# Performance work log

Hardware: AMD Instinct MI355X
Metric: run time of the kernel (lower is better)

## Reference

```python
import jax, jax.numpy as jnp
import numpy as np

B, S, D, N, TOPK = 2, 2048, 4096, 8, 2


def setup_inputs() -> dict:
    key = jax.random.key(0)
    k1, k2, k3, k4, k5 = jax.random.split(key, 5)
    return {
        "x": jax.random.normal(k1, (B, S, D), dtype=jnp.float32),
        "base_res": jax.random.normal(k2, (B, S, D), dtype=jnp.float32),
        "lora_results": jax.random.normal(k3, (B, S, D, N), dtype=jnp.float32),
        "gate_W": jax.random.normal(k4, (N, D), dtype=jnp.float32) * 0.02,
        "gate_b": jax.random.normal(k5, (N,), dtype=jnp.float32) * 0.02,
        "top_k": TOPK,
    }


def reference(x, base_res, lora_results, gate_W, gate_b, top_k):
    # Pool last token: [B, D]
    pooled = x[:, -1, :]
    # All per-adapter Linear(D,1) gates fused into one matmul: [B, N]
    gate_weights = jnp.einsum("bd,nd->bn", pooled, gate_W) + gate_b
    # Top-k adapter selection (add_noise=False / eval mode)
    _, adapter_index = jax.lax.top_k(gate_weights, top_k)  # [B, k]
    # Gather along adapter dim (dim 3): [B, S, D, k]
    idx = adapter_index[:, None, None, :]  # broadcast over S, D
    activated_res = jnp.take_along_axis(lora_results, idx, axis=3)
    # Sum over selected adapters and add residual (note: gate weights are NOT
    # multiplied in, matching the original module's math).
    return base_res + jnp.sum(activated_res, axis=-1)
```

## Files before the change

### kernel.cpp

```cpp
#include <hip/hip_runtime.h>
#include <hip/hip_bf16.h>

#define B_SZ 2
#define S_SZ 2048
#define D_SZ 4096
#define N_ADP 8

__global__ void moe_gate_topk(const float* __restrict__ x,
                              const float* __restrict__ gate_W,
                              const float* __restrict__ gate_b,
                              const int* __restrict__ top_k_p,
                              float* __restrict__ w_out) {
    const int b = blockIdx.x;
    const float* xrow = x + ((size_t)b * S_SZ + (S_SZ - 1)) * D_SZ;

    float acc[N_ADP];
#pragma unroll
    for (int n = 0; n < N_ADP; ++n) acc[n] = 0.f;

    for (int d = threadIdx.x; d < D_SZ; d += blockDim.x) {
        const float xv = xrow[d];
#pragma unroll
        for (int n = 0; n < N_ADP; ++n)
            acc[n] += xv * gate_W[n * D_SZ + d];
    }

#pragma unroll
    for (int n = 0; n < N_ADP; ++n) {
#pragma unroll
        for (int off = 32; off > 0; off >>= 1)
            acc[n] += __shfl_down(acc[n], off, 64);
    }

    __shared__ float red[N_ADP][4];
    const int wave = threadIdx.x >> 6;
    const int lane = threadIdx.x & 63;
    if (lane == 0) {
#pragma unroll
        for (int n = 0; n < N_ADP; ++n) red[n][wave] = acc[n];
    }
    __syncthreads();

    if (threadIdx.x == 0) {
        const int nwaves = (int)(blockDim.x >> 6);
        float g[N_ADP];
#pragma unroll
        for (int n = 0; n < N_ADP; ++n) {
            float s = 0.f;
            for (int w = 0; w < nwaves; ++w) s += red[n][w];
            g[n] = s + gate_b[n];
        }
        float wsel[N_ADP];
#pragma unroll
        for (int n = 0; n < N_ADP; ++n) wsel[n] = 0.f;

        const int k = *top_k_p;
        for (int t = 0; t < k && t < N_ADP; ++t) {
            int best = -1;
            float bv = 0.f;
            for (int n = 0; n < N_ADP; ++n) {
                if (wsel[n] == 0.f && (best < 0 || g[n] > bv)) {
                    bv = g[n];
                    best = n;
                }
            }
            wsel[best] = 1.f;
        }
#pragma unroll
        for (int n = 0; n < N_ADP; ++n) w_out[b * N_ADP + n] = wsel[n];
    }
}

__global__ void moe_aggregate(const float* __restrict__ base,
                              const float* __restrict__ lora,
                              const float* __restrict__ w_ws,
                              float* __restrict__ out) {
    const int b = blockIdx.y;

    const float w0 = w_ws[b * N_ADP + 0];
    const float w1 = w_ws[b * N_ADP + 1];
    const float w2 = w_ws[b * N_ADP + 2];
    const float w3 = w_ws[b * N_ADP + 3];
    const float w4 = w_ws[b * N_ADP + 4];
    const float w5 = w_ws[b * N_ADP + 5];
    const float w6 = w_ws[b * N_ADP + 6];
    const float w7 = w_ws[b * N_ADP + 7];

    const size_t batch_elems = (size_t)S_SZ * D_SZ;
    const size_t batch_off = (size_t)b * batch_elems;
    const int ngroups = (int)(batch_elems / 4);

    const int stride = gridDim.x * blockDim.x;
    for (int g = blockIdx.x * blockDim.x + threadIdx.x; g < ngroups; g += stride) {
        const size_t e = batch_off + (size_t)g * 4;
        const float4 bv = *reinterpret_cast<const float4*>(base + e);
        const float4* lp = reinterpret_cast<const float4*>(lora + e * N_ADP);

        float4 ov;
        float* ovp = reinterpret_cast<float*>(&ov);
        const float* bvp = reinterpret_cast<const float*>(&bv);
#pragma unroll
        for (int j = 0; j < 4; ++j) {
            const float4 l0 = lp[2 * j];
            const float4 l1 = lp[2 * j + 1];
            float s = bvp[j];
            s += w0 * l0.x + w1 * l0.y + w2 * l0.z + w3 * l0.w;
            s += w4 * l1.x + w5 * l1.y + w6 * l1.z + w7 * l1.w;
            ovp[j] = s;
        }
        *reinterpret_cast<float4*>(out + e) = ov;
    }
}

extern "C" void kernel_launch(void* const* d_in, const int* in_sizes, int n_in,
                              void* d_out, int out_size, void* d_ws, size_t ws_size,
                              hipStream_t stream) {
    const float* x        = (const float*)d_in[0];
    const float* base_res = (const float*)d_in[1];
    const float* lora     = (const float*)d_in[2];
    const float* gate_W   = (const float*)d_in[3];
    const float* gate_b   = (const float*)d_in[4];
    const int*   top_k    = (const int*)d_in[5];
    float* out = (float*)d_out;
    float* w_ws = (float*)d_ws;

    moe_gate_topk<<<dim3(B_SZ), dim3(256), 0, stream>>>(x, gate_W, gate_b, top_k, w_ws);

    dim3 grid(2048, B_SZ);
    moe_aggregate<<<grid, dim3(256), 0, stream>>>(base_res, lora, w_ws, out);
}
```

Measured before the change: 143.1 us.

## Coalesce lora loads via per-wave LDS transpose with XOR swizzle

The aggregate kernel now has each wave load a contiguous 8 KB tile of lora with fully coalesced float4 loads. It stages the tile through a swizzled LDS buffer, then each lane reads back its 8 float4s to produce one output float4. Before, each lane read 128 contiguous bytes, which gave strided per-instruction access. The change also shrinks the grid to 512x2 and doubles the gate kernel block size with unrolling. It adds LDS traffic and per-wave staging, and the overall kernel stays bound by DRAM bandwidth.

```diff
diff --git a/kernel.cpp b/kernel.cpp
--- a/kernel.cpp
+++ b/kernel.cpp
@@ -18,6 +18,7 @@
 #pragma unroll
     for (int n = 0; n < N_ADP; ++n) acc[n] = 0.f;
 
+#pragma unroll 4
     for (int d = threadIdx.x; d < D_SZ; d += blockDim.x) {
         const float xv = xrow[d];
 #pragma unroll
@@ -32,7 +33,7 @@
             acc[n] += __shfl_down(acc[n], off, 64);
     }
 
-    __shared__ float red[N_ADP][4];
+    __shared__ float red[N_ADP][8];
     const int wave = threadIdx.x >> 6;
     const int lane = threadIdx.x & 63;
     if (lane == 0) {
@@ -71,44 +72,60 @@
     }
 }
 
-__global__ void moe_aggregate(const float* __restrict__ base,
-                              const float* __restrict__ lora,
-                              const float* __restrict__ w_ws,
-                              float* __restrict__ out) {
+__global__ __launch_bounds__(256) void moe_aggregate(
+        const float4* __restrict__ base4,
+        const float4* __restrict__ lora4,
+        const float* __restrict__ w_ws,
+        float4* __restrict__ out4) {
+    __shared__ float4 lds[4][512];
+
+    const int wv = threadIdx.x >> 6;
+    const int lane = threadIdx.x & 63;
     const int b = blockIdx.y;
 
-    const float w0 = w_ws[b * N_ADP + 0];
-    const float w1 = w_ws[b * N_ADP + 1];
-    const float w2 = w_ws[b * N_ADP + 2];
-    const float w3 = w_ws[b * N_ADP + 3];
-    const float w4 = w_ws[b * N_ADP + 4];
-    const float w5 = w_ws[b * N_ADP + 5];
-    const float w6 = w_ws[b * N_ADP + 6];
-    const float w7 = w_ws[b * N_ADP + 7];
+    const float* wp = w_ws + b * N_ADP;
+    const float w0 = wp[0], w1 = wp[1], w2 = wp[2], w3 = wp[3];
+    const float w4 = wp[4], w5 = wp[5], w6 = wp[6], w7 = wp[7];
 
-    const size_t batch_elems = (size_t)S_SZ * D_SZ;
-    const size_t batch_off = (size_t)b * batch_elems;
-    const int ngroups = (int)(batch_elems / 4);
+    const size_t loraq_batch = (size_t)S_SZ * D_SZ * (N_ADP / 4);
+    const size_t outq_batch  = (size_t)S_SZ * D_SZ / 4;
+    const float4* lbase = lora4 + (size_t)b * loraq_batch;
+    const float4* bbase = base4 + (size_t)b * outq_batch;
+    float4*       obase = out4  + (size_t)b * outq_batch;
 
-    const int stride = gridDim.x * blockDim.x;
-    for (int g = blockIdx.x * blockDim.x + threadIdx.x; g < ngroups; g += stride) {
-        const size_t e = batch_off + (size_t)g * 4;
-        const float4 bv = *reinterpret_cast<const float4*>(base + e);
-        const float4* lp = reinterpret_cast<const float4*>(lora + e * N_ADP);
+    const int tiles   = (int)(loraq_batch / 512);
+    const int wstride = gridDim.x * 4;
+
+    for (int t = blockIdx.x * 4 + wv; t < tiles; t += wstride) {
+        const size_t qbase = (size_t)t * 512;
+
+        float4 v[8];
+#pragma unroll
+        for (int r = 0; r < 8; ++r)
+            v[r] = lbase[qbase + (size_t)r * 64 + lane];
+
+#pragma unroll
+        for (int r = 0; r < 8; ++r)
+            lds[wv][(r * 64 + lane) ^ ((lane >> 3) & 7)] = v[r];
+
+        const size_t o = qbase / 8 + lane;
+        const float4 bv = bbase[o];
+
+        float4 q[8];
+#pragma unroll
+        for (int j = 0; j < 8; ++j)
+            q[j] = lds[wv][(8 * lane + j) ^ (lane & 7)];
 
         float4 ov;
-        float* ovp = reinterpret_cast<float*>(&ov);
-        const float* bvp = reinterpret_cast<const float*>(&bv);
-#pragma unroll
-        for (int j = 0; j < 4; ++j) {
-            const float4 l0 = lp[2 * j];
-            const float4 l1 = lp[2 * j + 1];
-            float s = bvp[j];
-            s += w0 * l0.x + w1 * l0.y + w2 * l0.z + w3 * l0.w;
-            s += w4 * l1.x + w5 * l1.y + w6 * l1.z + w7 * l1.w;
-            ovp[j] = s;
-        }
-        *reinterpret_cast<float4*>(out + e) = ov;
+        ov.x = bv.x + w0 * q[0].x + w1 * q[0].y + w2 * q[0].z + w3 * q[0].w
+                    + w4 * q[1].x + w5 * q[1].y + w6 * q[1].z + w7 * q[1].w;
+        ov.y = bv.y + w0 * q[2].x + w1 * q[2].y + w2 * q[2].z + w3 * q[2].w
+                    + w4 * q[3].x + w5 * q[3].y + w6 * q[3].z + w7 * q[3].w;
+        ov.z = bv.z + w0 * q[4].x + w1 * q[4].y + w2 * q[4].z + w3 * q[4].w
+                    + w4 * q[5].x + w5 * q[5].y + w6 * q[5].z + w7 * q[5].w;
+        ov.w = bv.w + w0 * q[6].x + w1 * q[6].y + w2 * q[6].z + w3 * q[6].w
+                    + w4 * q[7].x + w5 * q[7].y + w6 * q[7].z + w7 * q[7].w;
+        obase[o] = ov;
     }
 }
 
@@ -121,11 +138,12 @@
     const float* gate_W   = (const float*)d_in[3];
     const float* gate_b   = (const float*)d_in[4];
     const int*   top_k    = (const int*)d_in[5];
-    float* out = (float*)d_out;
+    float* out  = (float*)d_out;
     float* w_ws = (float*)d_ws;
 
-    moe_gate_topk<<<dim3(B_SZ), dim3(256), 0, stream>>>(x, gate_W, gate_b, top_k, w_ws);
+    moe_gate_topk<<<dim3(B_SZ), dim3(512), 0, stream>>>(x, gate_W, gate_b, top_k, w_ws);
 
-    dim3 grid(2048, B_SZ);
-    moe_aggregate<<<grid, dim3(256), 0, stream>>>(base_res, lora, w_ws, out);
+    dim3 grid(512, B_SZ);
+    moe_aggregate<<<grid, dim3(256), 0, stream>>>(
+        (const float4*)base_res, (const float4*)lora, w_ws, (float4*)out);
 }
```

Result: no change. 141.0 us (-1.5%).

## Parallelize gate dot per adapter, move top-k into aggregate, use nontemporal loads

Applied to the files above, without the earlier changes.

The gate kernel now runs one block per (adapter, batch) pair with float4 loads, so the serial 2-block gate launch gets more parallelism. Top-k selection moves into each aggregate thread, which reads the raw gate scores and bias from the workspace. The aggregate kernel uses nontemporal loads and stores for the streaming lora, base and output tensors, with half the grid and launch bounds. It still reads all 8 adapters' data densely, and every thread redundantly recomputes the top-k.

```diff
diff --git a/kernel.cpp b/kernel.cpp
--- a/kernel.cpp
+++ b/kernel.cpp
@@ -6,109 +6,97 @@
 #define D_SZ 4096
 #define N_ADP 8
 
-__global__ void moe_gate_topk(const float* __restrict__ x,
-                              const float* __restrict__ gate_W,
-                              const float* __restrict__ gate_b,
-                              const int* __restrict__ top_k_p,
-                              float* __restrict__ w_out) {
-    const int b = blockIdx.x;
-    const float* xrow = x + ((size_t)b * S_SZ + (S_SZ - 1)) * D_SZ;
+typedef float f4_t __attribute__((ext_vector_type(4)));
 
-    float acc[N_ADP];
+__global__ void moe_gate_dot(const f4_t* __restrict__ x4,
+                             const f4_t* __restrict__ gateW4,
+                             float* __restrict__ g_out) {
+    const int n = blockIdx.x;
+    const int b = blockIdx.y;
+    const f4_t* xrow = x4 + ((size_t)b * S_SZ + (S_SZ - 1)) * (D_SZ / 4);
+    const f4_t* wrow = gateW4 + (size_t)n * (D_SZ / 4);
+
+    float s = 0.f;
 #pragma unroll
-    for (int n = 0; n < N_ADP; ++n) acc[n] = 0.f;
-
-    for (int d = threadIdx.x; d < D_SZ; d += blockDim.x) {
-        const float xv = xrow[d];
-#pragma unroll
-        for (int n = 0; n < N_ADP; ++n)
-            acc[n] += xv * gate_W[n * D_SZ + d];
+    for (int i = 0; i < D_SZ / 4 / 256; ++i) {
+        const int d4 = i * 256 + threadIdx.x;
+        const f4_t xv = xrow[d4];
+        const f4_t wv = wrow[d4];
+        s += xv.x * wv.x + xv.y * wv.y + xv.z * wv.z + xv.w * wv.w;
     }
 
 #pragma unroll
-    for (int n = 0; n < N_ADP; ++n) {
-#pragma unroll
-        for (int off = 32; off > 0; off >>= 1)
-            acc[n] += __shfl_down(acc[n], off, 64);
-    }
+    for (int off = 32; off > 0; off >>= 1)
+        s += __shfl_down(s, off, 64);
 
-    __shared__ float red[N_ADP][4];
+    __shared__ float red[4];
     const int wave = threadIdx.x >> 6;
     const int lane = threadIdx.x & 63;
-    if (lane == 0) {
+    if (lane == 0) red[wave] = s;
+    __syncthreads();
+    if (threadIdx.x == 0)
+        g_out[b * N_ADP + n] = red[0] + red[1] + red[2] + red[3];
+}
+
+__global__ __launch_bounds__(256, 4) void moe_aggregate(
+        const f4_t* __restrict__ base4,
+        const f4_t* __restrict__ lora4,
+        const float* __restrict__ g_ws,
+        const float* __restrict__ gate_b,
+        const int* __restrict__ top_k_p,
+        f4_t* __restrict__ out4) {
+    const int b = blockIdx.y;
+
+    float g[N_ADP];
 #pragma unroll
-        for (int n = 0; n < N_ADP; ++n) red[n][wave] = acc[n];
-    }
-    __syncthreads();
+    for (int n = 0; n < N_ADP; ++n) g[n] = g_ws[b * N_ADP + n] + gate_b[n];
 
-    if (threadIdx.x == 0) {
-        const int nwaves = (int)(blockDim.x >> 6);
-        float g[N_ADP];
+    float w[N_ADP];
 #pragma unroll
-        for (int n = 0; n < N_ADP; ++n) {
-            float s = 0.f;
-            for (int w = 0; w < nwaves; ++w) s += red[n][w];
-            g[n] = s + gate_b[n];
-        }
-        float wsel[N_ADP];
-#pragma unroll
-        for (int n = 0; n < N_ADP; ++n) wsel[n] = 0.f;
-
+    for (int n = 0; n < N_ADP; ++n) w[n] = 0.f;
+    {
         const int k = *top_k_p;
         for (int t = 0; t < k && t < N_ADP; ++t) {
             int best = -1;
             float bv = 0.f;
+#pragma unroll
             for (int n = 0; n < N_ADP; ++n) {
-                if (wsel[n] == 0.f && (best < 0 || g[n] > bv)) {
+                if (w[n] == 0.f && (best < 0 || g[n] > bv)) {
                     bv = g[n];
                     best = n;
                 }
             }
-            wsel[best] = 1.f;
+            w[best] = 1.f;
         }
-#pragma unroll
-        for (int n = 0; n < N_ADP; ++n) w_out[b * N_ADP + n] = wsel[n];
     }
-}
+    const float w0 = w[0], w1 = w[1], w2 = w[2], w3 = w[3];
+    const float w4 = w[4], w5 = w[5], w6 = w[6], w7 = w[7];
 
-__global__ void moe_aggregate(const float* __restrict__ base,
-                              const float* __restrict__ lora,
-                              const float* __restrict__ w_ws,
-                              float* __restrict__ out) {
-    const int b = blockIdx.y;
-
-    const float w0 = w_ws[b * N_ADP + 0];
-    const float w1 = w_ws[b * N_ADP + 1];
-    const float w2 = w_ws[b * N_ADP + 2];
-    const float w3 = w_ws[b * N_ADP + 3];
-    const float w4 = w_ws[b * N_ADP + 4];
-    const float w5 = w_ws[b * N_ADP + 5];
-    const float w6 = w_ws[b * N_ADP + 6];
-    const float w7 = w_ws[b * N_ADP + 7];
-
-    const size_t batch_elems = (size_t)S_SZ * D_SZ;
-    const size_t batch_off = (size_t)b * batch_elems;
-    const int ngroups = (int)(batch_elems / 4);
+    const size_t outq_batch = (size_t)S_SZ * D_SZ / 4;
+    const size_t obase_off = (size_t)b * outq_batch;
+    const int nq = (int)outq_batch;
 
     const int stride = gridDim.x * blockDim.x;
-    for (int g = blockIdx.x * blockDim.x + threadIdx.x; g < ngroups; g += stride) {
-        const size_t e = batch_off + (size_t)g * 4;
-        const float4 bv = *reinterpret_cast<const float4*>(base + e);
-        const float4* lp = reinterpret_cast<const float4*>(lora + e * N_ADP);
+    for (int q = blockIdx.x * blockDim.x + threadIdx.x; q < nq; q += stride) {
+        const size_t o = obase_off + (size_t)q;
+        const f4_t bv = __builtin_nontemporal_load(base4 + o);
+        const f4_t* lp = lora4 + o * N_ADP;
 
-        float4 ov;
-        float* ovp = reinterpret_cast<float*>(&ov);
-        const float* bvp = reinterpret_cast<const float*>(&bv);
+        f4_t l[8];
 #pragma unroll
-        for (int j = 0; j < 4; ++j) {
-            const float4 l0 = lp[2 * j];
-            const float4 l1 = lp[2 * j + 1];
-            float s = bvp[j];
-            s += w0 * l0.x + w1 * l0.y + w2 * l0.z + w3 * l0.w;
-            s += w4 * l1.x + w5 * l1.y + w6 * l1.z + w7 * l1.w;
-            ovp[j] = s;
-        }
-        *reinterpret_cast<float4*>(out + e) = ov;
+        for (int j = 0; j < 8; ++j)
+            l[j] = __builtin_nontemporal_load(lp + j);
+
+        f4_t ov;
+        ov.x = bv.x + w0 * l[0].x + w1 * l[0].y + w2 * l[0].z + w3 * l[0].w
+                    + w4 * l[1].x + w5 * l[1].y + w6 * l[1].z + w7 * l[1].w;
+        ov.y = bv.y + w0 * l[2].x + w1 * l[2].y + w2 * l[2].z + w3 * l[2].w
+                    + w4 * l[3].x + w5 * l[3].y + w6 * l[3].z + w7 * l[3].w;
+        ov.z = bv.z + w0 * l[4].x + w1 * l[4].y + w2 * l[4].z + w3 * l[4].w
+                    + w4 * l[5].x + w5 * l[5].y + w6 * l[5].z + w7 * l[5].w;
+        ov.w = bv.w + w0 * l[6].x + w1 * l[6].y + w2 * l[6].z + w3 * l[6].w
+                    + w4 * l[7].x + w5 * l[7].y + w6 * l[7].z + w7 * l[7].w;
+        __builtin_nontemporal_store(ov, out4 + o);
     }
 }
 
@@ -121,11 +109,13 @@
     const float* gate_W   = (const float*)d_in[3];
     const float* gate_b   = (const float*)d_in[4];
     const int*   top_k    = (const int*)d_in[5];
-    float* out = (float*)d_out;
-    float* w_ws = (float*)d_ws;
+    float* out  = (float*)d_out;
+    float* g_ws = (float*)d_ws;
 
-    moe_gate_topk<<<dim3(B_SZ), dim3(256), 0, stream>>>(x, gate_W, gate_b, top_k, w_ws);
+    moe_gate_dot<<<dim3(N_ADP, B_SZ), dim3(256), 0, stream>>>(
+        (const f4_t*)x, (const f4_t*)gate_W, g_ws);
 
-    dim3 grid(2048, B_SZ);
-    moe_aggregate<<<grid, dim3(256), 0, stream>>>(base_res, lora, w_ws, out);
+    moe_aggregate<<<dim3(1024, B_SZ), dim3(256), 0, stream>>>(
+        (const f4_t*)base_res, (const f4_t*)lora, g_ws, gate_b, top_k,
+        (f4_t*)out);
 }
```

New measurement: 255.8 us. +78.8%, slower.
